# Kernel optimization log

Hardware: AMD Instinct MI355X
Metric: run time of the kernel (lower is better)

Reference implementation:

```python
import jax, jax.numpy as jnp
import numpy as np

N = 100000
E = 3200000
IN_DIM = 128
OUT_DIM = 64


def setup_inputs() -> dict:
    key = jax.random.key(0)
    k1, k2, k3, k4, k5, k6 = jax.random.split(key, 6)
    x = jax.random.normal(k1, (N, IN_DIM), dtype=jnp.float32)
    edge_index = jax.random.randint(k2, (2, E), 0, N, dtype=jnp.int64)
    edge_weight = jax.random.uniform(k3, (E,), dtype=jnp.float32)
    # Learned params: Linear weight (in->out, no bias), attention vectors a_src/a_tgt
    limit_w = float(np.sqrt(1.0 / IN_DIM))
    W = jax.random.uniform(k4, (IN_DIM, OUT_DIM), minval=-limit_w, maxval=limit_w, dtype=jnp.float32)
    # xavier_uniform for (out_dim, 1) parameters
    limit_a = float(np.sqrt(6.0 / (OUT_DIM + 1)))
    a_src = jax.random.uniform(k5, (OUT_DIM,), minval=-limit_a, maxval=limit_a, dtype=jnp.float32)
    a_tgt = jax.random.uniform(k6, (OUT_DIM,), minval=-limit_a, maxval=limit_a, dtype=jnp.float32)
    return {"x": x, "edge_index": edge_index, "edge_weight": edge_weight,
            "W": W, "a_src": a_src, "a_tgt": a_tgt}


def reference(x, edge_index, edge_weight, W, a_src, a_tgt):
    n = x.shape[0]
    h = x @ W  # (N, out_dim)
    src, tgt = edge_index[0], edge_index[1]
    # per-node attention logits, gathered per edge
    hs = h @ a_src  # (N,)
    ht = h @ a_tgt  # (N,)
    e = jax.nn.leaky_relu(hs[src] + ht[tgt], negative_slope=0.2)  # (E,)
    e = e * edge_weight
    # segment softmax over incoming edges of each target node
    e_max = jax.ops.segment_max(e, tgt, num_segments=n)  # (N,), -inf for isolated nodes
    e_exp = jnp.exp(e - e_max[tgt])  # (E,)
    e_sum = jax.ops.segment_sum(e_exp, tgt, num_segments=n)  # (N,)
    alpha = e_exp / (e_sum[tgt] + 1e-10)  # (E,)
    # weighted scatter-add aggregation
    out = jax.ops.segment_sum(alpha[:, None] * h[src], tgt, num_segments=n)  # (N, out_dim)
    return out
```

## Files before the change

### kernel.cpp

```cpp
#include <hip/hip_runtime.h>


#define IN_DIM 128
#define OUT_DIM 64
#define LNODES 64
#define MAXBKT 512
#define BKN 256
#define EPT 8
#define BIN_CHUNK (512 * EPT)
#define CAP 9216

__device__ __forceinline__ unsigned short f2bf(float f) {
    unsigned u = __float_as_uint(f);
    return (unsigned short)((u + 0x7FFFu + ((u >> 16) & 1u)) >> 16);
}
__device__ __forceinline__ float bf2f(unsigned short u) {
    return __uint_as_float((unsigned)u << 16);
}

__device__ __forceinline__ float expg(float d) {
    return __expf(fmaxf(d, -80.f));
}

__global__ void k_init(int* __restrict__ bfill, int nbkt)
{
    int i = blockIdx.x * blockDim.x + threadIdx.x;
    if (i < nbkt) bfill[i] = i * CAP;
}

__global__ __launch_bounds__(512) void k_linear(
    const float* __restrict__ x, const float* __restrict__ W,
    const float* __restrict__ a_src, const float* __restrict__ a_tgt,
    unsigned short* __restrict__ hh, float* __restrict__ hs,
    float* __restrict__ ht, int n)
{
    __shared__ float ws_W[IN_DIM][OUT_DIM];
    __shared__ float xs[LNODES][IN_DIM + 4];
    const int tid   = threadIdx.x;
    const int node0 = blockIdx.x * LNODES;

    {
        const float4* Wsrc = (const float4*)W;
        float4* Wdst = (float4*)&ws_W[0][0];
        #pragma unroll
        for (int i = 0; i < 4; ++i) Wdst[tid + 512 * i] = Wsrc[tid + 512 * i];
    }
    {
        int nrows = n - node0; if (nrows > LNODES) nrows = LNODES;
        for (int i = tid; i < nrows * 32; i += 512) {
            int r = i >> 5, c4 = i & 31;
            float4 v = ((const float4*)(x + (size_t)(node0 + r) * IN_DIM))[c4];
            *(float4*)&xs[r][c4 * 4] = v;
        }
    }
    __syncthreads();

    const int lane16 = tid & 15;
    const int mrow   = tid >> 4;
    float4 acc[2];
    acc[0] = make_float4(0.f, 0.f, 0.f, 0.f);
    acc[1] = make_float4(0.f, 0.f, 0.f, 0.f);

    #pragma unroll 2
    for (int k = 0; k < IN_DIM; k += 4) {
        float4 w0 = *(const float4*)&ws_W[k + 0][lane16 * 4];
        float4 w1 = *(const float4*)&ws_W[k + 1][lane16 * 4];
        float4 w2 = *(const float4*)&ws_W[k + 2][lane16 * 4];
        float4 w3 = *(const float4*)&ws_W[k + 3][lane16 * 4];
        #pragma unroll
        for (int u = 0; u < 2; ++u) {
            float4 xv = *(const float4*)&xs[mrow + 32 * u][k];
            acc[u].x += w0.x * xv.x + w1.x * xv.y + w2.x * xv.z + w3.x * xv.w;
            acc[u].y += w0.y * xv.x + w1.y * xv.y + w2.y * xv.z + w3.y * xv.w;
            acc[u].z += w0.z * xv.x + w1.z * xv.y + w2.z * xv.z + w3.z * xv.w;
            acc[u].w += w0.w * xv.x + w1.w * xv.y + w2.w * xv.z + w3.w * xv.w;
        }
    }

    const float4 as = ((const float4*)a_src)[lane16];
    const float4 at = ((const float4*)a_tgt)[lane16];
    #pragma unroll
    for (int u = 0; u < 2; ++u) {
        int node = node0 + mrow + 32 * u;
        float ps = acc[u].x * as.x + acc[u].y * as.y + acc[u].z * as.z + acc[u].w * as.w;
        float pt = acc[u].x * at.x + acc[u].y * at.y + acc[u].z * at.z + acc[u].w * at.w;
        #pragma unroll
        for (int off = 8; off; off >>= 1) {
            ps += __shfl_xor(ps, off);
            pt += __shfl_xor(pt, off);
        }
        if (node < n) {
            ushort4 hv;
            hv.x = f2bf(acc[u].x); hv.y = f2bf(acc[u].y);
            hv.z = f2bf(acc[u].z); hv.w = f2bf(acc[u].w);
            ((ushort4*)(hh + (size_t)node * OUT_DIM))[lane16] = hv;
            if (lane16 == 0) { hs[node] = ps; ht[node] = pt; }
        }
    }
}

__global__ __launch_bounds__(512) void k_bin(
    const int* __restrict__ src, const int* __restrict__ tgt,
    const float* __restrict__ ew, const float* __restrict__ hs,
    const float* __restrict__ ht, int* __restrict__ bfill,
    float2* __restrict__ ecoarse, int ecount, int nbkt)
{
    __shared__ int h[MAXBKT];
    __shared__ int base[MAXBKT];
    const int tid = threadIdx.x;
    const int e0  = blockIdx.x * BIN_CHUNK;

    for (int i = tid; i < nbkt; i += 512) h[i] = 0;

    int   sreg[EPT], treg[EPT];
    float wreg[EPT];
    #pragma unroll
    for (int k = 0; k < EPT; ++k) {
        int j = e0 + k * 512 + tid;
        bool valid = j < ecount;
        sreg[k] = valid ? src[j] : 0;
        treg[k] = valid ? tgt[j] : 0;
        wreg[k] = valid ? ew[j]  : 0.f;
    }
    float hsr[EPT], htr[EPT];
    #pragma unroll
    for (int k = 0; k < EPT; ++k) hsr[k] = hs[sreg[k]];
    #pragma unroll
    for (int k = 0; k < EPT; ++k) htr[k] = ht[treg[k]];

    __syncthreads();

    int rank[EPT];
    #pragma unroll
    for (int k = 0; k < EPT; ++k) {
        int j = e0 + k * 512 + tid;
        if (j < ecount) rank[k] = atomicAdd(&h[treg[k] >> 8], 1);
    }
    __syncthreads();

    for (int i = tid; i < nbkt; i += 512) {
        int c = h[i];
        base[i] = c ? atomicAdd(&bfill[i], c) : 0;
    }
    __syncthreads();

    #pragma unroll
    for (int k = 0; k < EPT; ++k) {
        int j = e0 + k * 512 + tid;
        if (j < ecount) {
            float v = hsr[k] + htr[k];
            v = (v > 0.f) ? v : 0.2f * v;
            v *= wreg[k];
            unsigned key = ((unsigned)sreg[k] << 8) | ((unsigned)treg[k] & 255u);
            ecoarse[base[treg[k] >> 8] + rank[k]] = make_float2(__uint_as_float(key), v);
        }
    }
}

__global__ __launch_bounds__(1024, 8) void k_bucket(
    const int* __restrict__ bfill, const float2* __restrict__ ecoarse,
    const unsigned short* __restrict__ hh, float* __restrict__ out, int n)
{
    __shared__ float2 recs[CAP];
    __shared__ int   cnt[BKN];
    __shared__ int   pos0[BKN];
    __shared__ int   fill[BKN];
    __shared__ float mf[BKN];
    __shared__ float rden[BKN];

    const int tid   = threadIdx.x;
    const int bkt   = blockIdx.x;
    const int base  = bkt * CAP;
    const int node0 = bkt << 8;
    const int mcnt  = bfill[bkt] - base;

    for (int i = tid; i < BKN; i += 1024) cnt[i] = 0;
    __syncthreads();

    for (int j = tid; j < mcnt; j += 1024) {
        unsigned k = __float_as_uint(ecoarse[base + j].x);
        atomicAdd(&cnt[k & 255u], 1);
    }
    __syncthreads();

    if (tid < BKN) pos0[tid] = cnt[tid];
    __syncthreads();
    for (int off = 1; off < BKN; off <<= 1) {
        int u = 0;
        if (tid < BKN && tid >= off) u = pos0[tid - off];
        __syncthreads();
        if (tid < BKN) pos0[tid] += u;
        __syncthreads();
    }
    if (tid < BKN) fill[tid] = pos0[tid] - cnt[tid];
    __syncthreads();
    if (tid < BKN) pos0[tid] = fill[tid];
    __syncthreads();

    for (int j = tid; j < mcnt; j += 1024) {
        float2 e = ecoarse[base + j];
        unsigned k = __float_as_uint(e.x);
        int p = atomicAdd(&fill[k & 255u], 1);
        recs[p] = e;
    }
    __syncthreads();

    {
        const int G   = tid >> 4;
        const int l16 = tid & 15;
        #pragma unroll
        for (int r = 0; r < 4; ++r) {
            int tl = G + 64 * r;
            int s0 = pos0[tl], c = cnt[tl];
            float m = -INFINITY, s = 0.f;
            for (int j = l16; j < c; j += 16) {
                float v = recs[s0 + j].y;
                float nm = fmaxf(m, v);
                s = s * expg(m - nm) + expg(v - nm);
                m = nm;
            }
            #pragma unroll
            for (int off = 8; off; off >>= 1) {
                float mo = __shfl_xor(m, off);
                float so = __shfl_xor(s, off);
                float nm = fmaxf(m, mo);
                s = s * expg(m - nm) + so * expg(mo - nm);
                m = nm;
            }
            if (l16 == 0) { mf[tl] = m; rden[tl] = 1.f / (s + 1e-10f); }
        }
    }
    __syncthreads();

    const int lane = tid & 63;
    const int wv   = tid >> 6;
    const int g    = lane >> 4;
    const int l4   = lane & 15;
    #pragma unroll 1
    for (int r = 0; r < 16; ++r) {
        int tl = wv + 16 * r;
        int node = node0 + tl;
        if (node >= n) continue;
        int s0 = pos0[tl], e_ = s0 + cnt[tl];
        float m = mf[tl], rd = rden[tl];
        float4 a0 = make_float4(0.f, 0.f, 0.f, 0.f);
        float4 a1 = make_float4(0.f, 0.f, 0.f, 0.f);
        int j = s0;
        for (; j + 8 <= e_; j += 8) {
            float2 e0 = recs[j + g];
            float2 e1 = recs[j + 4 + g];
            int sA = (int)(__float_as_uint(e0.x) >> 8);
            int sB = (int)(__float_as_uint(e1.x) >> 8);
            ushort4 u0 = ((const ushort4*)(hh + (size_t)sA * OUT_DIM))[l4];
            ushort4 u1 = ((const ushort4*)(hh + (size_t)sB * OUT_DIM))[l4];
            float c0 = __expf(e0.y - m) * rd;
            float c1 = __expf(e1.y - m) * rd;
            a0.x += c0 * bf2f(u0.x); a0.y += c0 * bf2f(u0.y);
            a0.z += c0 * bf2f(u0.z); a0.w += c0 * bf2f(u0.w);
            a1.x += c1 * bf2f(u1.x); a1.y += c1 * bf2f(u1.y);
            a1.z += c1 * bf2f(u1.z); a1.w += c1 * bf2f(u1.w);
        }
        for (; j < e_; j += 4) {
            int jj = j + g;
            bool valid = jj < e_;
            float2 ed = recs[valid ? jj : (e_ - 1)];
            int sidx = (int)(__float_as_uint(ed.x) >> 8);
            ushort4 uv = ((const ushort4*)(hh + (size_t)sidx * OUT_DIM))[l4];
            float c = valid ? __expf(ed.y - m) * rd : 0.f;
            a0.x += c * bf2f(uv.x); a0.y += c * bf2f(uv.y);
            a0.z += c * bf2f(uv.z); a0.w += c * bf2f(uv.w);
        }
        a0.x += a1.x; a0.y += a1.y; a0.z += a1.z; a0.w += a1.w;

        #pragma unroll
        for (int off = 32; off >= 16; off >>= 1) {
            a0.x += __shfl_xor(a0.x, off);
            a0.y += __shfl_xor(a0.y, off);
            a0.z += __shfl_xor(a0.z, off);
            a0.w += __shfl_xor(a0.w, off);
        }
        if (g == 0)
            ((float4*)(out + (size_t)node * OUT_DIM))[l4] = a0;
    }
}

extern "C" void kernel_launch(void* const* d_in, const int* in_sizes, int n_in,
                              void* d_out, int out_size, void* d_ws, size_t ws_size,
                              hipStream_t stream) {
    const float* x     = (const float*)d_in[0];
    const int*   eidx  = (const int*)d_in[1];
    const float* ew    = (const float*)d_in[2];
    const float* W     = (const float*)d_in[3];
    const float* a_src = (const float*)d_in[4];
    const float* a_tgt = (const float*)d_in[5];
    float* out = (float*)d_out;

    const int n = in_sizes[0] / IN_DIM;
    const int E = in_sizes[2];
    const int* src = eidx;
    const int* tgt = eidx + E;
    const int nbkt = (n + BKN - 1) / BKN;

    unsigned* ws = (unsigned*)d_ws;
    unsigned short* hh = (unsigned short*)ws;  ws += (size_t)n * OUT_DIM / 2;
    float* hs     = (float*)ws;          ws += n;
    float* ht     = (float*)ws;          ws += n;
    int*   bfill  = (int*)ws;            ws += MAXBKT;
    ws = (unsigned*)(((uintptr_t)ws + 7) & ~(uintptr_t)7);
    float2* ecoarse = (float2*)ws;

    k_init<<<1, 512, 0, stream>>>(bfill, nbkt);
    k_linear<<<(n + LNODES - 1) / LNODES, 512, 0, stream>>>(x, W, a_src, a_tgt, hh, hs, ht, n);
    k_bin<<<(E + BIN_CHUNK - 1) / BIN_CHUNK, 512, 0, stream>>>(src, tgt, ew, hs, ht, bfill, ecoarse, E, nbkt);
    k_bucket<<<nbkt, 1024, 0, stream>>>(bfill, ecoarse, hh, out, n);
}
```

Measured before the change: 268.6 us.

## Replace global atomic bucket fill with count, column-scan, scatter passes

Measured after the change: 271.6 us. Within noise of the previous version (+1.1%).

```diff
diff --git a/kernel.cpp b/kernel.cpp
--- a/kernel.cpp
+++ b/kernel.cpp
@@ -6,8 +6,8 @@
 #define LNODES 64
 #define MAXBKT 512
 #define BKN 256
-#define EPT 8
-#define BIN_CHUNK (512 * EPT)
+#define SEPT 8
+#define SCHUNK (1024 * SEPT)
 #define CAP 9216
 
 __device__ __forceinline__ unsigned short f2bf(float f) {
@@ -20,12 +20,6 @@
 
 __device__ __forceinline__ float expg(float d) {
     return __expf(fmaxf(d, -80.f));
-}
-
-__global__ void k_init(int* __restrict__ bfill, int nbkt)
-{
-    int i = blockIdx.x * blockDim.x + threadIdx.x;
-    if (i < nbkt) bfill[i] = i * CAP;
 }
 
 __global__ __launch_bounds__(512) void k_linear(
@@ -99,60 +93,94 @@
     }
 }
 
-__global__ __launch_bounds__(512) void k_bin(
+__global__ __launch_bounds__(1024) void k_count(
+    const int* __restrict__ tgt, int* __restrict__ histT,
+    int ecount, int nbkt, int nsb)
+{
+    __shared__ int h[MAXBKT];
+    const int tid = threadIdx.x;
+    const int e0  = blockIdx.x * SCHUNK;
+    for (int i = tid; i < nbkt; i += 1024) h[i] = 0;
+    __syncthreads();
+    #pragma unroll
+    for (int k = 0; k < SEPT; ++k) {
+        int j = e0 + k * 1024 + tid;
+        if (j < ecount) atomicAdd(&h[tgt[j] >> 8], 1);
+    }
+    __syncthreads();
+    for (int i = tid; i < nbkt; i += 1024) histT[i * nsb + blockIdx.x] = h[i];
+}
+
+__global__ __launch_bounds__(512) void k_colscan(
+    int* __restrict__ histT, int* __restrict__ bfill, int nsb)
+{
+    __shared__ int lds[512];
+    const int bkt = blockIdx.x;
+    const int tid = threadIdx.x;
+    int v = (tid < nsb) ? histT[bkt * nsb + tid] : 0;
+    lds[tid] = v;
+    __syncthreads();
+    for (int off = 1; off < 512; off <<= 1) {
+        int u = (tid >= off) ? lds[tid - off] : 0;
+        __syncthreads();
+        lds[tid] += u;
+        __syncthreads();
+    }
+    int excl = lds[tid] - v;
+    if (tid < nsb) histT[bkt * nsb + tid] = bkt * CAP + excl;
+    if (tid == 511) bfill[bkt] = bkt * CAP + lds[511];
+}
+
+__global__ __launch_bounds__(1024) void k_scat(
     const int* __restrict__ src, const int* __restrict__ tgt,
     const float* __restrict__ ew, const float* __restrict__ hs,
-    const float* __restrict__ ht, int* __restrict__ bfill,
-    float2* __restrict__ ecoarse, int ecount, int nbkt)
+    const float* __restrict__ ht, const int* __restrict__ histT,
+    float2* __restrict__ ecoarse, int ecount, int nbkt, int nsb)
 {
     __shared__ int h[MAXBKT];
     __shared__ int base[MAXBKT];
     const int tid = threadIdx.x;
-    const int e0  = blockIdx.x * BIN_CHUNK;
-
-    for (int i = tid; i < nbkt; i += 512) h[i] = 0;
-
-    int   sreg[EPT], treg[EPT];
-    float wreg[EPT];
-    #pragma unroll
-    for (int k = 0; k < EPT; ++k) {
-        int j = e0 + k * 512 + tid;
+    const int e0  = blockIdx.x * SCHUNK;
+
+    for (int i = tid; i < nbkt; i += 1024) {
+        h[i] = 0;
+        base[i] = histT[i * nsb + blockIdx.x];
+    }
+
+    unsigned kreg[SEPT]; int breg[SEPT]; float wreg[SEPT];
+    #pragma unroll
+    for (int k = 0; k < SEPT; ++k) {
+        int j = e0 + k * 1024 + tid;
         bool valid = j < ecount;
-        sreg[k] = valid ? src[j] : 0;
-        treg[k] = valid ? tgt[j] : 0;
-        wreg[k] = valid ? ew[j]  : 0.f;
-    }
-    float hsr[EPT], htr[EPT];
-    #pragma unroll
-    for (int k = 0; k < EPT; ++k) hsr[k] = hs[sreg[k]];
-    #pragma unroll
-    for (int k = 0; k < EPT; ++k) htr[k] = ht[treg[k]];
-
-    __syncthreads();
-
-    int rank[EPT];
-    #pragma unroll
-    for (int k = 0; k < EPT; ++k) {
-        int j = e0 + k * 512 + tid;
-        if (j < ecount) rank[k] = atomicAdd(&h[treg[k] >> 8], 1);
-    }
-    __syncthreads();
-
-    for (int i = tid; i < nbkt; i += 512) {
-        int c = h[i];
-        base[i] = c ? atomicAdd(&bfill[i], c) : 0;
-    }
-    __syncthreads();
-
-    #pragma unroll
-    for (int k = 0; k < EPT; ++k) {
-        int j = e0 + k * 512 + tid;
+        int s = valid ? src[j] : 0;
+        int t = valid ? tgt[j] : 0;
+        wreg[k] = valid ? ew[j] : 0.f;
+        kreg[k] = ((unsigned)s << 8) | ((unsigned)t & 255u);
+        breg[k] = t >> 8;
+    }
+    float hsr[SEPT], htr[SEPT];
+    #pragma unroll
+    for (int k = 0; k < SEPT; ++k) hsr[k] = hs[kreg[k] >> 8];
+    #pragma unroll
+    for (int k = 0; k < SEPT; ++k) htr[k] = ht[(breg[k] << 8) | (int)(kreg[k] & 255u)];
+
+    __syncthreads();
+
+    int rank[SEPT];
+    #pragma unroll
+    for (int k = 0; k < SEPT; ++k) {
+        int j = e0 + k * 1024 + tid;
+        if (j < ecount) rank[k] = atomicAdd(&h[breg[k]], 1);
+    }
+
+    #pragma unroll
+    for (int k = 0; k < SEPT; ++k) {
+        int j = e0 + k * 1024 + tid;
         if (j < ecount) {
             float v = hsr[k] + htr[k];
             v = (v > 0.f) ? v : 0.2f * v;
             v *= wreg[k];
-            unsigned key = ((unsigned)sreg[k] << 8) | ((unsigned)treg[k] & 255u);
-            ecoarse[base[treg[k] >> 8] + rank[k]] = make_float2(__uint_as_float(key), v);
+            ecoarse[base[breg[k]] + rank[k]] = make_float2(__uint_as_float(kreg[k]), v);
         }
     }
 }
@@ -300,17 +328,20 @@
     const int* src = eidx;
     const int* tgt = eidx + E;
     const int nbkt = (n + BKN - 1) / BKN;
+    const int nsb  = (E + SCHUNK - 1) / SCHUNK;
 
     unsigned* ws = (unsigned*)d_ws;
     unsigned short* hh = (unsigned short*)ws;  ws += (size_t)n * OUT_DIM / 2;
     float* hs     = (float*)ws;          ws += n;
     float* ht     = (float*)ws;          ws += n;
     int*   bfill  = (int*)ws;            ws += MAXBKT;
+    int*   histT  = (int*)ws;            ws += (size_t)nbkt * nsb;
     ws = (unsigned*)(((uintptr_t)ws + 7) & ~(uintptr_t)7);
     float2* ecoarse = (float2*)ws;
 
-    k_init<<<1, 512, 0, stream>>>(bfill, nbkt);
     k_linear<<<(n + LNODES - 1) / LNODES, 512, 0, stream>>>(x, W, a_src, a_tgt, hh, hs, ht, n);
-    k_bin<<<(E + BIN_CHUNK - 1) / BIN_CHUNK, 512, 0, stream>>>(src, tgt, ew, hs, ht, bfill, ecoarse, E, nbkt);
+    k_count<<<nsb, 1024, 0, stream>>>(tgt, histT, E, nbkt, nsb);
+    k_colscan<<<nbkt, 512, 0, stream>>>(histT, bfill, nsb);
+    k_scat<<<nsb, 1024, 0, stream>>>(src, tgt, ew, hs, ht, histT, ecoarse, E, nbkt, nsb);
     k_bucket<<<nbkt, 1024, 0, stream>>>(bfill, ecoarse, hh, out, n);
 }
```
